# Optimization experiments

Measured on AMD Instinct MI355X. Metric: run time of the kernel, lower is better.

Reference implementation:

```python
import jax, jax.numpy as jnp
import numpy as np

IN_F, OUT_F, GS = 4096, 11008, 128


def setup_inputs() -> dict:
    key = jax.random.key(0)
    k1, k2, k3, k4 = jax.random.split(key, 4)
    x = jax.random.normal(k1, (4, 2048, IN_F), dtype=jnp.float32)
    # int8-valued weights stored in int32 container, as in the module
    weight = jax.random.randint(k2, (OUT_F, IN_F), -128, 128, dtype=jnp.int32)
    # scales in [...,0] (kept positive-ish), zeros in [...,1]
    scales = jax.random.uniform(k3, (IN_F // GS, OUT_F, 1), dtype=jnp.float32, minval=0.001, maxval=0.02)
    zeros = jax.random.normal(k4, (IN_F // GS, OUT_F, 1), dtype=jnp.float32) * 0.1
    scales_and_zeros = jnp.concatenate([scales, zeros], axis=-1)
    bias = jax.random.normal(jax.random.fold_in(key, 7), (OUT_F,), dtype=jnp.float32) * 0.02
    return {"x": x, "weight": weight, "scales_and_zeros": scales_and_zeros, "bias": bias, "group_size": GS}


def reference(x, weight, scales_and_zeros, bias, group_size):
    O, I = weight.shape
    G = I // group_size
    orig_shape = x.shape
    x2 = x.reshape(-1, I)                                   # [N, I]
    scales = scales_and_zeros[:, :, 0]                      # [G, O]
    zeros = scales_and_zeros[:, :, 1]                       # [G, O]
    # per-group dequant: w_fp[o, g, j] = q * scale[g, o] + zero[g, o]
    wq = weight.reshape(O, G, group_size).astype(x.dtype)   # [O, G, gs]
    w_fp = wq * scales.T[:, :, None] + zeros.T[:, :, None]  # [O, G, gs]
    w_fp = w_fp.reshape(O, I)
    y = x2 @ w_fp.T + bias                                  # [N, O]
    return y.reshape(*orig_shape[:-1], O)
```

## Files before the change

kernel.cpp:

```cpp
#include <hip/hip_runtime.h>
#include <stdint.h>

#define DEVFN __device__ __forceinline__

constexpr int M_DIM = 8192;
constexpr int K_DIM = 4096;
constexpr int N_DIM = 11008;
constexpr int GS = 128;
constexpr int NGROUPS = K_DIM / GS;

typedef __bf16 bf16_t;
typedef bf16_t bf16x8 __attribute__((ext_vector_type(8)));
typedef float f32x4 __attribute__((ext_vector_type(4)));

DEVFN ushort f2bf(float f) {
  uint32_t u = __builtin_bit_cast(uint32_t, f);
  u += 0x7fffu + ((u >> 16) & 1u);
  return (ushort)(u >> 16);
}

__global__ __launch_bounds__(256) void k_cvt_x(const float* __restrict__ x,
                                               ushort* __restrict__ out) {
  const size_t i4 = (size_t)blockIdx.x * 256 + threadIdx.x;
  const float4 v = ((const float4*)x)[i4];
  ushort4 r;
  r.x = f2bf(v.x); r.y = f2bf(v.y); r.z = f2bf(v.z); r.w = f2bf(v.w);
  ((ushort4*)out)[i4] = r;
}

__global__ __launch_bounds__(256) void k_dequant_w(const int* __restrict__ w,
                                                   const float* __restrict__ snz,
                                                   ushort* __restrict__ out) {
  const size_t i4 = (size_t)blockIdx.x * 256 + threadIdx.x;
  const size_t idx = i4 * 4;
  const int o = (int)(idx >> 12);
  const int i = (int)(idx & 4095);
  const int g = i >> 7;
  const float2 sz = ((const float2*)snz)[(size_t)g * N_DIM + o];
  const int4 wv = ((const int4*)w)[i4];
  ushort4 r;
  r.x = f2bf((float)wv.x * sz.x + sz.y);
  r.y = f2bf((float)wv.y * sz.x + sz.y);
  r.z = f2bf((float)wv.z * sz.x + sz.y);
  r.w = f2bf((float)wv.w * sz.x + sz.y);
  ((ushort4*)out)[i4] = r;
}

constexpr int BM = 128, BN = 128, BK = 32;
constexpr int NBN = N_DIM / BN;
constexpr int NBM = M_DIM / BM;
constexpr int KITERS = K_DIM / BK;

DEVFN void gload_lds16(const ushort* g, ushort* l) {
  __builtin_amdgcn_global_load_lds(
      (const __attribute__((address_space(1))) void*)g,
      (__attribute__((address_space(3))) void*)l,
      16, 0, 0);
}

__global__ __launch_bounds__(256) void k_gemm(const ushort* __restrict__ A,
                                              const ushort* __restrict__ B,
                                              const float* __restrict__ bias,
                                              float* __restrict__ C) {
  __shared__ __align__(16) ushort As[BM * BK];
  __shared__ __align__(16) ushort Bs[BN * BK];

  const int tid = threadIdx.x;
  const int wave = tid >> 6;
  const int lane = tid & 63;

  const int bid = blockIdx.x;
  const int xcd = bid & 7;
  const int local = bid >> 3;
  const int bm = xcd * 8 + (local & 7);
  const int bn = local >> 3;

  const int c0 = wave * 2;
  const int srow = c0 * 16 + (lane >> 2);
  const int skoff = (lane & 3) * 8;
  const ushort* ag0 = A + (size_t)(bm * BM + srow) * K_DIM + skoff;
  const ushort* ag1 = ag0 + (size_t)16 * K_DIM;
  const ushort* bg0 = B + (size_t)(bn * BN + srow) * K_DIM + skoff;
  const ushort* bg1 = bg0 + (size_t)16 * K_DIM;
  ushort* la0 = &As[c0 * 512];
  ushort* la1 = la0 + 512;
  ushort* lb0 = &Bs[c0 * 512];
  ushort* lb1 = lb0 + 512;

  const int wm = (wave & 1) * 64;
  const int wn = (wave >> 1) * 64;
  const int fr = lane & 15;
  const int quad = lane >> 4;
  const ushort* pa = &As[(wm + fr) * BK + quad * 8];
  const ushort* pb = &Bs[(wn + fr) * BK + quad * 8];

  f32x4 acc[4][4] = {};

  for (int kt = 0; kt < KITERS; ++kt) {
    const int k0 = kt * BK;
    gload_lds16(ag0 + k0, la0);
    gload_lds16(ag1 + k0, la1);
    gload_lds16(bg0 + k0, lb0);
    gload_lds16(bg1 + k0, lb1);
    __syncthreads();

    bf16x8 af[4], bfr[4];
#pragma unroll
    for (int i = 0; i < 4; ++i) {
      af[i]  = *(const bf16x8*)(pa + i * 16 * BK);
      bfr[i] = *(const bf16x8*)(pb + i * 16 * BK);
    }
#pragma unroll
    for (int mi = 0; mi < 4; ++mi)
#pragma unroll
      for (int ni = 0; ni < 4; ++ni)
        acc[mi][ni] = __builtin_amdgcn_mfma_f32_16x16x32_bf16(
            af[mi], bfr[ni], acc[mi][ni], 0, 0, 0);
    __syncthreads();
  }

  const int row0 = bm * BM + wm + quad * 4;
  const int col0 = bn * BN + wn + fr;
#pragma unroll
  for (int ni = 0; ni < 4; ++ni) {
    const int col = col0 + ni * 16;
    const float bv = bias[col];
#pragma unroll
    for (int mi = 0; mi < 4; ++mi) {
      float* cp = C + (size_t)(row0 + mi * 16) * N_DIM + col;
#pragma unroll
      for (int r = 0; r < 4; ++r)
        cp[(size_t)r * N_DIM] = acc[mi][ni][r] + bv;
    }
  }
}

__global__ __launch_bounds__(256) void k_naive(const float* __restrict__ x,
                                               const int* __restrict__ w,
                                               const float* __restrict__ snz,
                                               const float* __restrict__ bias,
                                               float* __restrict__ y) {
  const int o = blockIdx.x * 256 + threadIdx.x;
  const int m = blockIdx.y;
  const float* xr = x + (size_t)m * K_DIM;
  const int* wr = w + (size_t)o * K_DIM;
  float acc = 0.f;
  for (int g = 0; g < NGROUPS; ++g) {
    const float2 sz = ((const float2*)snz)[(size_t)g * N_DIM + o];
    float pd = 0.f, px = 0.f;
    const int base = g * GS;
    for (int i = 0; i < GS; i += 4) {
      float4 xv = *(const float4*)(xr + base + i);
      int4 wv = *(const int4*)(wr + base + i);
      pd += xv.x * wv.x + xv.y * wv.y + xv.z * wv.z + xv.w * wv.w;
      px += xv.x + xv.y + xv.z + xv.w;
    }
    acc += sz.x * pd + sz.y * px;
  }
  y[(size_t)m * N_DIM + o] = acc + bias[o];
}

extern "C" void kernel_launch(void* const* d_in, const int* in_sizes, int n_in,
                              void* d_out, int out_size, void* d_ws, size_t ws_size,
                              hipStream_t stream) {
  const float* x    = (const float*)d_in[0];
  const int*   w    = (const int*)d_in[1];
  const float* snz  = (const float*)d_in[2];
  const float* bias = (const float*)d_in[3];
  float* out = (float*)d_out;

  const size_t wbytes = (size_t)N_DIM * K_DIM * 2;
  const size_t xbytes = (size_t)M_DIM * K_DIM * 2;

  if (ws_size >= wbytes + xbytes) {
    ushort* wbf = (ushort*)d_ws;
    ushort* xbf = (ushort*)((char*)d_ws + wbytes);
    k_cvt_x<<<dim3(32768), dim3(256), 0, stream>>>(x, xbf);
    k_dequant_w<<<dim3(44032), dim3(256), 0, stream>>>(w, snz, wbf);
    k_gemm<<<dim3(NBM * NBN), dim3(256), 0, stream>>>(xbf, wbf, bias, out);
  } else {
    k_naive<<<dim3(N_DIM / 256, M_DIM), dim3(256), 0, stream>>>(x, w, snz, bias, out);
  }
}
```

Baseline: 1.401 ms.

## Replace GEMM with 256x256 tile, 8-wave ping-pong pipelined kernel

Replaces the 128x128 single-buffered bf16 GEMM with a 256x256x64 tile kernel using 512 threads. The kernel double-buffers A/B halves in 128KB LDS with XOR-swizzled layout, interleaves async global-to-LDS loads with MFMA blocks under fine-grained barriers and vmcnt waits, and raises wave priority during MFMA. It is meant to raise arithmetic intensity, hide global load latency and avoid LDS bank conflicts. In exchange it uses the full LDS per workgroup and keeps many accumulators in registers, which limits occupancy, and its hand-tuned waitcnt and barrier schedule carries correctness risk.

```diff
diff --git a/kernel.cpp b/kernel.cpp
--- a/kernel.cpp
+++ b/kernel.cpp
@@ -46,91 +46,168 @@
   ((ushort4*)out)[i4] = r;
 }
 
-constexpr int BM = 128, BN = 128, BK = 32;
-constexpr int NBN = N_DIM / BN;
-constexpr int NBM = M_DIM / BM;
-constexpr int KITERS = K_DIM / BK;
-
-DEVFN void gload_lds16(const ushort* g, ushort* l) {
+constexpr int BM2 = 256, BN2 = 256, BK2 = 64;
+constexpr int NBM2 = M_DIM / BM2;
+constexpr int NBN2 = N_DIM / BN2;
+constexpr int KT2 = K_DIM / BK2;
+constexpr int NWG2 = NBM2 * NBN2;
+
+#define BAR() __builtin_amdgcn_s_barrier()
+#define LGKM0() asm volatile("s_waitcnt lgkmcnt(0)" ::: "memory")
+#define VMC4() asm volatile("s_waitcnt vmcnt(4)" ::: "memory")
+#define VMC0() asm volatile("s_waitcnt vmcnt(0)" ::: "memory")
+
+DEVFN void gld16(const ushort* g, ushort* l) {
   __builtin_amdgcn_global_load_lds(
       (const __attribute__((address_space(1))) void*)g,
-      (__attribute__((address_space(3))) void*)l,
-      16, 0, 0);
-}
-
-__global__ __launch_bounds__(256) void k_gemm(const ushort* __restrict__ A,
-                                              const ushort* __restrict__ B,
-                                              const float* __restrict__ bias,
-                                              float* __restrict__ C) {
-  __shared__ __align__(16) ushort As[BM * BK];
-  __shared__ __align__(16) ushort Bs[BN * BK];
+      (__attribute__((address_space(3))) void*)l, 16, 0, 0);
+}
+
+DEVFN void stage_half(const ushort* gbase, int h, int kt, ushort* lp) {
+  const ushort* s = gbase + (size_t)(h * 128) * K_DIM + kt * 64;
+  gld16(s, lp);
+  gld16(s + (size_t)64 * K_DIM, lp + 4096);
+}
+
+template <int H>
+DEVFN void lda(const ushort* p0, const ushort* p1, bf16x8 (&af)[4][2]) {
+#pragma unroll
+  for (int mi = 0; mi < 4; ++mi) {
+    af[mi][0] = *(const bf16x8*)(p0 + (H * 4 + mi) * 1024);
+    af[mi][1] = *(const bf16x8*)(p1 + (H * 4 + mi) * 1024);
+  }
+}
+template <int P>
+DEVFN void ldb(const ushort* p0, const ushort* p1, bf16x8 (&bv)[4][2]) {
+#pragma unroll
+  for (int q = 0; q < 2; ++q) {
+    bv[P * 2 + q][0] = *(const bf16x8*)(p0 + (P * 2 + q) * 1024);
+    bv[P * 2 + q][1] = *(const bf16x8*)(p1 + (P * 2 + q) * 1024);
+  }
+}
+template <int H, int P>
+DEVFN void mm16(f32x4 (&acc)[8][4], const bf16x8 (&af)[4][2], const bf16x8 (&bv)[4][2]) {
+#pragma unroll
+  for (int kk = 0; kk < 2; ++kk)
+#pragma unroll
+    for (int mi = 0; mi < 4; ++mi)
+#pragma unroll
+      for (int ni = 0; ni < 2; ++ni)
+        acc[H * 4 + mi][P * 2 + ni] = __builtin_amdgcn_mfma_f32_16x16x32_bf16(
+            af[mi][kk], bv[P * 2 + ni][kk], acc[H * 4 + mi][P * 2 + ni], 0, 0, 0);
+}
+
+__global__ __launch_bounds__(512) void k_gemm256(const ushort* __restrict__ A,
+                                                 const ushort* __restrict__ B,
+                                                 const float* __restrict__ bias,
+                                                 float* __restrict__ C) {
+  __shared__ __align__(16) ushort smem[65536];
 
   const int tid = threadIdx.x;
   const int wave = tid >> 6;
   const int lane = tid & 63;
-
-  const int bid = blockIdx.x;
-  const int xcd = bid & 7;
-  const int local = bid >> 3;
-  const int bm = xcd * 8 + (local & 7);
-  const int bn = local >> 3;
-
-  const int c0 = wave * 2;
-  const int srow = c0 * 16 + (lane >> 2);
-  const int skoff = (lane & 3) * 8;
-  const ushort* ag0 = A + (size_t)(bm * BM + srow) * K_DIM + skoff;
-  const ushort* ag1 = ag0 + (size_t)16 * K_DIM;
-  const ushort* bg0 = B + (size_t)(bn * BN + srow) * K_DIM + skoff;
-  const ushort* bg1 = bg0 + (size_t)16 * K_DIM;
-  ushort* la0 = &As[c0 * 512];
-  ushort* la1 = la0 + 512;
-  ushort* lb0 = &Bs[c0 * 512];
-  ushort* lb1 = lb0 + 512;
-
-  const int wm = (wave & 1) * 64;
-  const int wn = (wave >> 1) * 64;
+  const int wm = wave >> 2;
+  const int wn = wave & 3;
   const int fr = lane & 15;
   const int quad = lane >> 4;
-  const ushort* pa = &As[(wm + fr) * BK + quad * 8];
-  const ushort* pb = &Bs[(wn + fr) * BK + quad * 8];
-
-  f32x4 acc[4][4] = {};
-
-  for (int kt = 0; kt < KITERS; ++kt) {
-    const int k0 = kt * BK;
-    gload_lds16(ag0 + k0, la0);
-    gload_lds16(ag1 + k0, la1);
-    gload_lds16(bg0 + k0, lb0);
-    gload_lds16(bg1 + k0, lb1);
-    __syncthreads();
-
-    bf16x8 af[4], bfr[4];
-#pragma unroll
-    for (int i = 0; i < 4; ++i) {
-      af[i]  = *(const bf16x8*)(pa + i * 16 * BK);
-      bfr[i] = *(const bf16x8*)(pb + i * 16 * BK);
-    }
-#pragma unroll
-    for (int mi = 0; mi < 4; ++mi)
-#pragma unroll
-      for (int ni = 0; ni < 4; ++ni)
-        acc[mi][ni] = __builtin_amdgcn_mfma_f32_16x16x32_bf16(
-            af[mi], bfr[ni], acc[mi][ni], 0, 0, 0);
-    __syncthreads();
-  }
-
-  const int row0 = bm * BM + wm + quad * 4;
-  const int col0 = bn * BN + wn + fr;
+  const int frq = fr & 7;
+
+  const int bid = blockIdx.x;
+  const int wg = (bid & 7) * (NWG2 / 8) + (bid >> 3);
+  const int bm = wg / NBN2;
+  const int bn = wg - bm * NBN2;
+
+  const int ch0 = ((quad ^ frq) << 3);
+  const int ch1 = (((4 | quad) ^ frq) << 3);
+  const ushort* pA00 = smem + (wm * 128 + fr) * 64 + ch0;
+  const ushort* pA01 = smem + (wm * 128 + fr) * 64 + ch1;
+  const ushort* pA10 = pA00 + 32768;
+  const ushort* pA11 = pA01 + 32768;
+  const ushort* pB00 = smem + 16384 + (wn * 64 + fr) * 64 + ch0;
+  const ushort* pB01 = smem + 16384 + (wn * 64 + fr) * 64 + ch1;
+  const ushort* pB10 = pB00 + 32768;
+  const ushort* pB11 = pB01 + 32768;
+
+  const int srow = tid >> 3;
+  const int scol = ((tid & 7) ^ (srow & 7)) * 8;
+  const ushort* pAg = A + (size_t)(bm * 256 + srow) * K_DIM + scol;
+  const ushort* pBg = B + (size_t)(bn * 256 + srow) * K_DIM + scol;
+  ushort* const ws = smem + wave * 512;
+
+  f32x4 acc[8][4] = {};
+
+  stage_half(pAg, 0, 0, ws + 0);
+  stage_half(pAg, 1, 0, ws + 8192);
+  stage_half(pBg, 0, 0, ws + 16384);
+  stage_half(pBg, 1, 0, ws + 24576);
+  stage_half(pBg, 0, 1, ws + 49152);
+  stage_half(pBg, 1, 1, ws + 57344);
+  VMC4();
+  BAR();
+
+#pragma unroll 1
+  for (int it = 0; it < KT2 / 2; ++it) {
+    const int t1 = 2 * it + 1;
+    const int t2 = (2 * it + 2 < KT2) ? 2 * it + 2 : KT2 - 1;
+    const int t3 = (2 * it + 3 < KT2) ? 2 * it + 3 : KT2 - 1;
+    bf16x8 af[4][2], bv[4][2];
+    lda<0>(pA00, pA01, af);
+    ldb<0>(pB00, pB01, bv);
+    stage_half(pAg, 0, t1, ws + 32768);
+    BAR(); LGKM0();
+    __builtin_amdgcn_s_setprio(1); mm16<0, 0>(acc, af, bv); __builtin_amdgcn_s_setprio(0);
+    BAR();
+    ldb<1>(pB00, pB01, bv);
+    stage_half(pAg, 1, t1, ws + 40960);
+    BAR(); LGKM0();
+    __builtin_amdgcn_s_setprio(1); mm16<0, 1>(acc, af, bv); __builtin_amdgcn_s_setprio(0);
+    BAR();
+    lda<1>(pA00, pA01, af);
+    stage_half(pBg, 0, t2, ws + 16384);
+    BAR(); LGKM0();
+    __builtin_amdgcn_s_setprio(1); mm16<1, 1>(acc, af, bv); __builtin_amdgcn_s_setprio(0);
+    BAR();
+    stage_half(pBg, 1, t2, ws + 24576);
+    BAR();
+    __builtin_amdgcn_s_setprio(1); mm16<1, 0>(acc, af, bv); __builtin_amdgcn_s_setprio(0);
+    VMC4();
+    BAR();
+    lda<0>(pA10, pA11, af);
+    ldb<0>(pB10, pB11, bv);
+    stage_half(pAg, 0, t2, ws + 0);
+    BAR(); LGKM0();
+    __builtin_amdgcn_s_setprio(1); mm16<0, 0>(acc, af, bv); __builtin_amdgcn_s_setprio(0);
+    BAR();
+    ldb<1>(pB10, pB11, bv);
+    stage_half(pAg, 1, t2, ws + 8192);
+    BAR(); LGKM0();
+    __builtin_amdgcn_s_setprio(1); mm16<0, 1>(acc, af, bv); __builtin_amdgcn_s_setprio(0);
+    BAR();
+    lda<1>(pA10, pA11, af);
+    stage_half(pBg, 0, t3, ws + 49152);
+    BAR(); LGKM0();
+    __builtin_amdgcn_s_setprio(1); mm16<1, 1>(acc, af, bv); __builtin_amdgcn_s_setprio(0);
+    BAR();
+    stage_half(pBg, 1, t3, ws + 57344);
+    BAR();
+    __builtin_amdgcn_s_setprio(1); mm16<1, 0>(acc, af, bv); __builtin_amdgcn_s_setprio(0);
+    VMC4();
+    BAR();
+  }
+  VMC0();
+
+  const int row0 = bm * 256 + wm * 128 + quad * 4;
+  const int col0 = bn * 256 + wn * 64 + fr;
 #pragma unroll
   for (int ni = 0; ni < 4; ++ni) {
     const int col = col0 + ni * 16;
-    const float bv = bias[col];
-#pragma unroll
-    for (int mi = 0; mi < 4; ++mi) {
+    const float bvv = bias[col];
+#pragma unroll
+    for (int mi = 0; mi < 8; ++mi) {
       float* cp = C + (size_t)(row0 + mi * 16) * N_DIM + col;
 #pragma unroll
       for (int r = 0; r < 4; ++r)
-        cp[(size_t)r * N_DIM] = acc[mi][ni][r] + bv;
+        cp[(size_t)r * N_DIM] = acc[mi][ni][r] + bvv;
     }
   }
 }
@@ -177,7 +254,7 @@
     ushort* xbf = (ushort*)((char*)d_ws + wbytes);
     k_cvt_x<<<dim3(32768), dim3(256), 0, stream>>>(x, xbf);
     k_dequant_w<<<dim3(44032), dim3(256), 0, stream>>>(w, snz, wbf);
-    k_gemm<<<dim3(NBM * NBN), dim3(256), 0, stream>>>(xbf, wbf, bias, out);
+    k_gemm256<<<dim3(NWG2), dim3(512), 0, stream>>>(xbf, wbf, bias, out);
   } else {
     k_naive<<<dim3(N_DIM / 256, M_DIM), dim3(256), 0, stream>>>(x, w, snz, bias, out);
   }
```

New measurement: 1.155 ms. 17.6% less time.
